# Kernel optimization log

Hardware: AMD Instinct MI355X
Metric: run time of the kernel (lower is better)

The kernel has to match this reference:

```python
import jax, jax.numpy as jnp
import numpy as np
from jax import lax

B, IMG, P, C_IN, E, H, NAX = 128, 224, 16, 1, 96, 4, 14
N = NAX * NAX  # 196 patches


def _ln(x, g, b, axes=(-1,)):
    mu = jnp.mean(x, axes, keepdims=True)
    v = jnp.var(x, axes, keepdims=True)
    return (x - mu) * lax.rsqrt(v + 1e-5) * g + b


def _embed3d(p):
    # p: [B, N, E]. Torch code rotates pair (2i,2i+1) by theta_i*col (row loop)
    # then theta_i*row (col loop) in-place => total angle theta_i*(row+col).
    bsz = p.shape[0]
    f = p.transpose(0, 2, 1).reshape(bsz, E, NAX, NAX)
    i = jnp.arange(E // 2, dtype=jnp.float32)
    theta = 10000.0 ** (-2.0 * i / E)  # [48]
    pos = jnp.arange(NAX, dtype=jnp.float32)
    ang = theta[:, None, None] * (pos[None, :, None] + pos[None, None, :])  # [48,14,14]
    cos, sin = jnp.cos(ang), jnp.sin(ang)
    xe, ye = f[:, 0::2], f[:, 1::2]  # [B,48,14,14] each
    rx = xe * cos - ye * sin
    ry = xe * sin + ye * cos
    f = jnp.stack([rx, ry], axis=2).reshape(bsz, E, NAX, NAX)  # re-interleave pairs
    return f.reshape(bsz, E, N).transpose(0, 2, 1)


def _mhsa(x, g, bt, Wqkv, bqkv, Wo, bo):
    # standard pre-norm residual MHSA block (MHSelfAttentionBlock assumed)
    h = _ln(x, g, bt)
    qkv = h @ Wqkv + bqkv  # [B,N,3E]
    q, k, v = jnp.split(qkv, 3, axis=-1)
    d = E // H
    def heads(t):
        return t.reshape(t.shape[0], N, H, d).transpose(0, 2, 1, 3)  # [B,H,N,d]
    q, k, v = heads(q), heads(k), heads(v)
    s = jnp.einsum('bhqd,bhkd->bhqk', q, k) / jnp.sqrt(jnp.float32(d))
    a = jax.nn.softmax(s, axis=-1)
    o = jnp.einsum('bhqk,bhkd->bhqd', a, v).transpose(0, 2, 1, 3).reshape(x.shape[0], N, E)
    return x + o @ Wo + bo


def _convT(x, w, b):
    # torch ConvTranspose2d(k=4, s=2, p=1); w: [C_in, C_out, 4, 4]
    wt = jnp.transpose(jnp.flip(w, (2, 3)), (1, 0, 2, 3))  # OIHW, flipped
    y = lax.conv_general_dilated(x, wt, (1, 1), ((2, 2), (2, 2)), lhs_dilation=(2, 2),
                                 dimension_numbers=('NCHW', 'OIHW', 'NCHW'))
    return y + b[None, :, None, None]


def _forward(x, timestep, Wp, bp, Wt1, bt1, Wt2, bt2,
             a0_g, a0_b, a0_Wqkv, a0_bqkv, a0_Wo, a0_bo,
             a1_g, a1_b, a1_Wqkv, a1_bqkv, a1_Wo, a1_bo,
             Wm0, bm0, Wm1, bm1, Wm2, bm2,
             Wd1, bd1, l1g, l1b, Wd2, bd2, l2g, l2b, Wd3, bd3, l3g, l3b, Wd4, bd4):
    # timestep embedding: emb = -log(0.5)*t -> [sin, cos] -> MLP
    e = 0.6931471805599453 * timestep[0]
    tv = jnp.stack([jnp.sin(e), jnp.cos(e)])  # [2]
    time = jax.nn.silu(tv @ Wt1 + bt1) @ Wt2 + bt2  # [E]
    # patch embed: conv stride 16
    p = lax.conv_general_dilated(x, Wp, (P, P), 'VALID',
                                 dimension_numbers=('NCHW', 'OIHW', 'NCHW'))
    p = (p + bp[None, :, None, None]).reshape(x.shape[0], E, N).transpose(0, 2, 1)  # [B,N,E]
    p = _embed3d(p)
    p = _mhsa(p, a0_g, a0_b, a0_Wqkv, a0_bqkv, a0_Wo, a0_bo)
    p = _mhsa(p, a1_g, a1_b, a1_Wqkv, a1_bqkv, a1_Wo, a1_bo)
    p = p + time
    p = jax.nn.silu(p @ Wm0 + bm0)
    p = jax.nn.silu(p @ Wm1 + bm1)
    p = jax.nn.silu(p @ Wm2 + bm2)
    # unpatchify decoder
    f = p.transpose(0, 2, 1).reshape(x.shape[0], E, NAX, NAX)
    f = jax.nn.silu(_ln(_convT(f, Wd1, bd1), l1g, l1b, (-2, -1)))  # [B,48,28,28]
    f = jax.nn.silu(_ln(_convT(f, Wd2, bd2), l2g, l2b, (-2, -1)))  # [B,24,56,56]
    f = jax.nn.silu(_ln(_convT(f, Wd3, bd3), l3g, l3b, (-2, -1)))  # [B,12,112,112]
    f = jax.nn.silu(_convT(f, Wd4, bd4))                            # [B,1,224,224]
    return jnp.clip(f, 0.0, 1.0)


def setup_inputs() -> dict:
    ks = jax.random.split(jax.random.key(0), 40)
    rn = lambda k, s: (jax.random.normal(k, s, jnp.float32) * 0.02)
    inp = {
        'x': jax.random.normal(ks[0], (B, C_IN, IMG, IMG), jnp.float32),
        'timestep': jax.random.uniform(ks[1], (1,), jnp.float32),
        'Wp': rn(ks[2], (E, C_IN, P, P)), 'bp': jnp.zeros((E,), jnp.float32),
        'Wt1': rn(ks[3], (2, 128)), 'bt1': jnp.zeros((128,), jnp.float32),
        'Wt2': rn(ks[4], (128, E)), 'bt2': jnp.zeros((E,), jnp.float32),
        'a0_g': jnp.ones((E,), jnp.float32), 'a0_b': jnp.zeros((E,), jnp.float32),
        'a0_Wqkv': rn(ks[5], (E, 3 * E)), 'a0_bqkv': jnp.zeros((3 * E,), jnp.float32),
        'a0_Wo': rn(ks[6], (E, E)), 'a0_bo': jnp.zeros((E,), jnp.float32),
        'a1_g': jnp.ones((E,), jnp.float32), 'a1_b': jnp.zeros((E,), jnp.float32),
        'a1_Wqkv': rn(ks[7], (E, 3 * E)), 'a1_bqkv': jnp.zeros((3 * E,), jnp.float32),
        'a1_Wo': rn(ks[8], (E, E)), 'a1_bo': jnp.zeros((E,), jnp.float32),
        'Wm0': rn(ks[9], (E, E)), 'bm0': jnp.zeros((E,), jnp.float32),
        'Wm1': rn(ks[10], (E, E)), 'bm1': jnp.zeros((E,), jnp.float32),
        'Wm2': rn(ks[11], (E, E)), 'bm2': jnp.zeros((E,), jnp.float32),
        'Wd1': rn(ks[12], (E, 48, 4, 4)), 'bd1': jnp.zeros((48,), jnp.float32),
        'l1g': jnp.ones((28, 28), jnp.float32), 'l1b': jnp.zeros((28, 28), jnp.float32),
        'Wd2': rn(ks[13], (48, 24, 4, 4)), 'bd2': jnp.zeros((24,), jnp.float32),
        'l2g': jnp.ones((56, 56), jnp.float32), 'l2b': jnp.zeros((56, 56), jnp.float32),
        'Wd3': rn(ks[14], (24, 12, 4, 4)), 'bd3': jnp.zeros((12,), jnp.float32),
        'l3g': jnp.ones((112, 112), jnp.float32), 'l3b': jnp.zeros((112, 112), jnp.float32),
        'Wd4': rn(ks[15], (12, 1, 4, 4)), 'bd4': jnp.zeros((1,), jnp.float32),
    }
    return inp


def reference(x, timestep, Wp, bp, Wt1, bt1, Wt2, bt2,
              a0_g, a0_b, a0_Wqkv, a0_bqkv, a0_Wo, a0_bo,
              a1_g, a1_b, a1_Wqkv, a1_bqkv, a1_Wo, a1_bo,
              Wm0, bm0, Wm1, bm1, Wm2, bm2,
              Wd1, bd1, l1g, l1b, Wd2, bd2, l2g, l2b, Wd3, bd3, l3g, l3b, Wd4, bd4):
    return _forward(x, timestep, Wp, bp, Wt1, bt1, Wt2, bt2,
                    a0_g, a0_b, a0_Wqkv, a0_bqkv, a0_Wo, a0_bo,
                    a1_g, a1_b, a1_Wqkv, a1_bqkv, a1_Wo, a1_bo,
                    Wm0, bm0, Wm1, bm1, Wm2, bm2,
                    Wd1, bd1, l1g, l1b, Wd2, bd2, l2g, l2b, Wd3, bd3, l3g, l3b, Wd4, bd4)
```

## Files before the change

kernel.cpp:

```cpp
#include <hip/hip_runtime.h>
#include <cmath>


#define B_   128
#define NPATCH 196
#define M_ROWS (B_*NPATCH)
#define E_   96

typedef _Float16 half8 __attribute__((ext_vector_type(8)));
typedef _Float16 half4v __attribute__((ext_vector_type(4)));
typedef float f32x4 __attribute__((ext_vector_type(4)));

__global__ void k_time(const float* __restrict__ ts,
                       const float* __restrict__ Wt1, const float* __restrict__ bt1,
                       const float* __restrict__ Wt2, const float* __restrict__ bt2,
                       float* __restrict__ timev)
{
    __shared__ float h[128];
    float e = 0.69314718055994530942f * ts[0];
    float sv = sinf(e), cv = cosf(e);
    int t = threadIdx.x;
    float z = sv * Wt1[t] + cv * Wt1[128 + t] + bt1[t];
    h[t] = z / (1.f + expf(-z));
    __syncthreads();
    if (t < 96) {
        float acc = bt2[t];
        for (int j = 0; j < 128; ++j) acc += h[j] * Wt2[j * 96 + t];
        timev[t] = acc;
    }
}

__global__ void __launch_bounds__(256) k_zstat(float* __restrict__ stat)
{
    int i = blockIdx.x * 256 + threadIdx.x;
    if (i < 21504) stat[i] = 0.f;
}

__global__ void __launch_bounds__(256) k_repack(const float* __restrict__ w1,
                                                const float* __restrict__ w2,
                                                const float* __restrict__ w3,
                                                const float* __restrict__ w4f,
                                                float* __restrict__ wr)
{
    int i = blockIdx.x * 256 + threadIdx.x;
    const float* src; int CIN, COUT, e; float* dst;
    if      (i < 73728) { src = w1;  CIN = 96; COUT = 48; e = i;          dst = wr; }
    else if (i < 92160) { src = w2;  CIN = 48; COUT = 24; e = i - 73728;  dst = wr + 73728; }
    else if (i < 96768) { src = w3;  CIN = 24; COUT = 12; e = i - 92160;  dst = wr + 92160; }
    else if (i < 96960) { src = w4f; CIN = 12; COUT = 1;  e = i - 96768;  dst = wr + 96768; }
    else return;
    int per = CIN * COUT * 4;
    int par = e / per, rem = e % per;
    int ci = rem / (COUT * 4);
    int o  = (rem >> 2) % COUT;
    int j  = rem & 3;
    int ry = par >> 1, rx = par & 1;
    int wy = (j < 2)  ? (3 - ry) : (1 - ry);
    int wx = (j & 1)  ? (1 - rx) : (3 - rx);
    dst[e] = src[(ci * COUT + o) * 16 + wy * 4 + wx];
}

__global__ void __launch_bounds__(256) k_wcvtc(const float* __restrict__ w1,
                                               _Float16* __restrict__ wc)
{
    int i = blockIdx.x * 256 + threadIdx.x;
    if (i >= 4 * 48 * 384) return;
    int p = i / 18432, rem = i % 18432;
    int o = rem / 384, k = rem % 384;
    int tap = k / 96, ci = k % 96;
    int ry = p >> 1, rx = p & 1;
    int wy = (tap < 2) ? (3 - ry) : (1 - ry);
    int wx = (tap & 1) ? (1 - rx) : (3 - rx);
    wc[i] = (_Float16)w1[(ci * 48 + o) * 16 + wy * 4 + wx];
}

__global__ void __launch_bounds__(256) k_wcvt2(const float* __restrict__ w2,
                                               _Float16* __restrict__ wc2)
{
    int i = blockIdx.x * 256 + threadIdx.x;
    if (i >= 4 * 32 * 192) return;
    int p = i / 6144, rem = i % 6144;
    int o = rem / 192, k = rem % 192;
    int tap = k / 48, ci = k % 48;
    int ry = p >> 1, rx = p & 1;
    int wy = (tap < 2) ? (3 - ry) : (1 - ry);
    int wx = (tap & 1) ? (1 - rx) : (3 - rx);
    wc2[i] = (o < 24) ? (_Float16)w2[(ci * 24 + o) * 16 + wy * 4 + wx]
                      : (_Float16)0.f;
}

__global__ void __launch_bounds__(256) k_wcvt3(const float* __restrict__ w3,
                                               _Float16* __restrict__ wc3)
{
    int i = blockIdx.x * 256 + threadIdx.x;
    if (i >= 4 * 16 * 96) return;
    int p = i / 1536, rem = i % 1536;
    int o = rem / 96, k = rem % 96;
    int tap = k / 24, ci = k % 24;
    int ry = p >> 1, rx = p & 1;
    int wy = (tap < 2) ? (3 - ry) : (1 - ry);
    int wx = (tap & 1) ? (1 - rx) : (3 - rx);
    wc3[i] = (o < 12) ? (_Float16)w3[(ci * 12 + o) * 16 + wy * 4 + wx]
                      : (_Float16)0.f;
}

__global__ void __launch_bounds__(256) k_wcvt(const float* __restrict__ qkv0,
                                              const float* __restrict__ qkv1,
                                              const float* __restrict__ wo0,
                                              const float* __restrict__ wo1,
                                              const float* __restrict__ wm0,
                                              const float* __restrict__ wm1,
                                              const float* __restrict__ wm2,
                                              _Float16* __restrict__ wh)
{
    int i = blockIdx.x * 256 + threadIdx.x;
    const float* src; int N; int e;
    if      (i < 27648)  { src = qkv0; N = 288; e = i; }
    else if (i < 55296)  { src = qkv1; N = 288; e = i - 27648; }
    else if (i < 64512)  { src = wo0;  N = 96;  e = i - 55296; }
    else if (i < 73728)  { src = wo1;  N = 96;  e = i - 64512; }
    else if (i < 82944)  { src = wm0;  N = 96;  e = i - 73728; }
    else if (i < 92160)  { src = wm1;  N = 96;  e = i - 82944; }
    else if (i < 101376) { src = wm2;  N = 96;  e = i - 92160; }
    else return;
    int n = e / 96, k = e % 96;
    wh[i] = (_Float16)src[k * N + n];
}

__global__ void __launch_bounds__(256) k_zb_h(_Float16* __restrict__ xinh)
{
    int i = blockIdx.x * 256 + threadIdx.x;
    if (i >= 128 * 60 * 96) return;
    int b = i / 5760, r = i % 5760;
    int pos = r / 96, ch = r % 96;
    int py, px;
    if      (pos < 16) { py = 0;        px = pos; }
    else if (pos < 32) { py = 15;       px = pos - 16; }
    else if (pos < 46) { py = pos - 31; px = 0; }
    else               { py = pos - 45; px = 15; }
    xinh[((size_t)(b * 256) + py * 16 + px) * 96 + ch] = (_Float16)0.f;
}

__global__ void __launch_bounds__(256) k_patch_mfma(const float* __restrict__ x,
                                                    const float* __restrict__ Wp,
                                                    const float* __restrict__ bp,
                                                    float* __restrict__ out)
{
    __shared__ __align__(16) _Float16 Ah[64 * 136];
    __shared__ __align__(16) _Float16 Wh[96 * 136];
    int t = threadIdx.x;
    int p0 = blockIdx.x * 64;
    int wave = t >> 6, lane = t & 63;
    int lm = lane & 15, quad = lane >> 4;
    f32x4 acc[6];
    #pragma unroll
    for (int nt = 0; nt < 6; ++nt) acc[nt] = (f32x4){0.f, 0.f, 0.f, 0.f};

    for (int kc = 0; kc < 2; ++kc) {
        __syncthreads();
        for (int i = t; i < 512; i += 256) {
            int lp = i >> 3, pyl = i & 7;
            int patch = p0 + lp;
            int b = patch / NPATCH, n = patch % NPATCH;
            int ny = n / 14, nx = n % 14;
            const float4* s4 = (const float4*)(x +
                ((size_t)(b * 224) + ny * 16 + kc * 8 + pyl) * 224 + nx * 16);
            float4 v0 = s4[0], v1 = s4[1], v2 = s4[2], v3 = s4[3];
            half8 h0, h1;
            h0[0]=(_Float16)v0.x; h0[1]=(_Float16)v0.y; h0[2]=(_Float16)v0.z; h0[3]=(_Float16)v0.w;
            h0[4]=(_Float16)v1.x; h0[5]=(_Float16)v1.y; h0[6]=(_Float16)v1.z; h0[7]=(_Float16)v1.w;
            h1[0]=(_Float16)v2.x; h1[1]=(_Float16)v2.y; h1[2]=(_Float16)v2.z; h1[3]=(_Float16)v2.w;
            h1[4]=(_Float16)v3.x; h1[5]=(_Float16)v3.y; h1[6]=(_Float16)v3.z; h1[7]=(_Float16)v3.w;
            *(half8*)&Ah[lp * 136 + pyl * 16]     = h0;
            *(half8*)&Ah[lp * 136 + pyl * 16 + 8] = h1;
        }
        for (int i = t; i < 1536; i += 256) {
            int e = i >> 4, s = i & 15;
            const float4* s4 = (const float4*)(Wp + e * 256 + kc * 128 + s * 8);
            float4 v0 = s4[0], v1 = s4[1];
            half8 h0;
            h0[0]=(_Float16)v0.x; h0[1]=(_Float16)v0.y; h0[2]=(_Float16)v0.z; h0[3]=(_Float16)v0.w;
            h0[4]=(_Float16)v1.x; h0[5]=(_Float16)v1.y; h0[6]=(_Float16)v1.z; h0[7]=(_Float16)v1.w;
            *(half8*)&Wh[e * 136 + s * 8] = h0;
        }
        __syncthreads();
        half8 af[4];
        #pragma unroll
        for (int ks = 0; ks < 4; ++ks)
            af[ks] = *(const half8*)&Ah[(wave * 16 + lm) * 136 + ks * 32 + quad * 8];
        #pragma unroll
        for (int ks = 0; ks < 4; ++ks) {
            #pragma unroll
            for (int nt = 0; nt < 6; ++nt) {
                half8 bf = *(const half8*)&Wh[(nt * 16 + lm) * 136 + ks * 32 + quad * 8];
                acc[nt] = __builtin_amdgcn_mfma_f32_16x16x32_f16(af[ks], bf, acc[nt], 0, 0, 0);
            }
        }
    }

    #pragma unroll
    for (int nt = 0; nt < 6; ++nt) {
        #pragma unroll
        for (int r = 0; r < 4; ++r) {
            int e = nt * 16 + lm;
            int lp = wave * 16 + quad * 4 + r;
            int patch = p0 + lp;
            int n = patch % NPATCH;
            int ny = n / 14, nx = n % 14;
            float yx = (float)(ny + nx);
            float v = acc[nt][r] + bp[e];
            float other = __shfl_xor(v, 1);
            float fi = (float)(e >> 1);
            float theta = expf(fi * (-2.f / 96.f) * 9.210340371976184f);
            float ang = theta * yx;
            float c = cosf(ang), s = sinf(ang);
            float outv = (lm & 1) ? (other * s + v * c) : (v * c - other * s);
            out[(size_t)patch * 96 + e] = outv;
        }
    }
}

__global__ void __launch_bounds__(256) k_ln_row(const float* __restrict__ x,
                                                const float* __restrict__ g,
                                                const float* __restrict__ bv,
                                                _Float16* __restrict__ out, int M)
{
    int lane = threadIdx.x & 63;
    int gw = (blockIdx.x * 256 + threadIdx.x) >> 6;
    int nw = (gridDim.x * 256) >> 6;
    float g0 = g[lane], b0 = bv[lane];
    float g1 = 0.f, b1 = 0.f;
    if (lane < 32) { g1 = g[64 + lane]; b1 = bv[64 + lane]; }
    for (int r = gw; r < M; r += nw) {
        const float* xr = x + (size_t)r * 96;
        float a = xr[lane];
        float c = (lane < 32) ? xr[64 + lane] : 0.f;
        float s = a + c, q = a * a + c * c;
        #pragma unroll
        for (int off = 32; off; off >>= 1) {
            s += __shfl_xor(s, off);
            q += __shfl_xor(q, off);
        }
        float mu = s * (1.f / 96.f);
        float rstd = rsqrtf(q * (1.f / 96.f) - mu * mu + 1e-5f);
        _Float16* orow = out + (size_t)r * 96;
        orow[lane] = (_Float16)((a - mu) * rstd * g0 + b0);
        if (lane < 32) orow[64 + lane] = (_Float16)((c - mu) * rstd * g1 + b1);
    }
}

template<int NCHUNKS, int OUTMODE, bool SILU, bool RES, bool ADDTIME, bool AHALF>
__global__ void __launch_bounds__(256) k_gemm_mfma(const void* __restrict__ A,
                                                   const _Float16* __restrict__ Wt,
                                                   const float* __restrict__ bias,
                                                   const float* __restrict__ res,
                                                   const float* __restrict__ timev,
                                                   void* __restrict__ outp)
{
    __shared__ __align__(16) _Float16 Ah[64 * 96];
    __shared__ __align__(16) _Float16 Wh[96 * 96];
    constexpr int NTOT = NCHUNKS * 96;
    int t = threadIdx.x;
    size_t row0 = (size_t)blockIdx.x * 64;

    if constexpr (AHALF) {
        const uint4* a4 = (const uint4*)((const _Float16*)A + row0 * 96);
        uint4* dst = (uint4*)Ah;
        for (int i = t; i < 768; i += 256) dst[i] = a4[i];
    } else {
        const float4* a4 = (const float4*)((const float*)A + row0 * 96);
        for (int i = t; i < 1536; i += 256) {
            float4 v = a4[i];
            half4v hv;
            hv[0] = (_Float16)v.x; hv[1] = (_Float16)v.y;
            hv[2] = (_Float16)v.z; hv[3] = (_Float16)v.w;
            *(half4v*)&Ah[i * 4] = hv;
        }
    }

    int wave = t >> 6, lane = t & 63;
    int lm = lane & 15, quad = lane >> 4;
    const f32x4 vzero = {0.f, 0.f, 0.f, 0.f};

    for (int ch = blockIdx.y; ch < NCHUNKS; ch += gridDim.y) {
        __syncthreads();
        {
            const uint4* src = (const uint4*)(Wt + (size_t)ch * 9216);
            uint4* dst = (uint4*)Wh;
            for (int i = t; i < 1152; i += 256) dst[i] = src[i];
        }
        __syncthreads();

        half8 af[3];
        #pragma unroll
        for (int ks = 0; ks < 3; ++ks)
            af[ks] = *(const half8*)&Ah[(wave * 16 + lm) * 96 + ks * 32 + quad * 8];

        f32x4 acc[6];
        #pragma unroll
        for (int ct = 0; ct < 6; ++ct) acc[ct] = vzero;

        #pragma unroll
        for (int ct = 0; ct < 6; ++ct) {
            #pragma unroll
            for (int ks = 0; ks < 3; ++ks) {
                half8 bf = *(const half8*)&Wh[(ct * 16 + lm) * 96 + ks * 32 + quad * 8];
                acc[ct] = __builtin_amdgcn_mfma_f32_16x16x32_f16(af[ks], bf, acc[ct], 0, 0, 0);
            }
        }

        #pragma unroll
        for (int ct = 0; ct < 6; ++ct) {
            #pragma unroll
            for (int r = 0; r < 4; ++r) {
                int lr = wave * 16 + quad * 4 + r;
                size_t row = row0 + lr;
                int lc = ct * 16 + lm;
                int col = ch * 96 + lc;
                float v = acc[ct][r] + bias[col];
                if constexpr (RES)     v += res[row * 96 + lc];
                if constexpr (ADDTIME) v += timev[lc];
                if constexpr (SILU)    v = v / (1.f + __expf(-v));
                if constexpr (OUTMODE == 0) {
                    ((float*)outp)[row * NTOT + col] = v;
                } else {
                    ((_Float16*)outp)[row * NTOT + col] = (_Float16)v;
                }
            }
        }
    }
}

__global__ void __launch_bounds__(256) k_mlp_fused(const float* __restrict__ A,
                                                   const _Float16* __restrict__ W,
                                                   const float* __restrict__ b0,
                                                   const float* __restrict__ b1,
                                                   const float* __restrict__ b2,
                                                   _Float16* __restrict__ outh)
{
    __shared__ __align__(16) _Float16 Ah[2][64 * 96];
    __shared__ __align__(16) _Float16 Wh[3][96 * 96];
    int t = threadIdx.x;
    size_t row0 = (size_t)blockIdx.x * 64;

    const float4* a4 = (const float4*)(A + row0 * 96);
    for (int i = t; i < 1536; i += 256) {
        float4 v = a4[i];
        half4v hv;
        hv[0] = (_Float16)v.x; hv[1] = (_Float16)v.y;
        hv[2] = (_Float16)v.z; hv[3] = (_Float16)v.w;
        *(half4v*)&Ah[0][i * 4] = hv;
    }
    {
        const uint4* src = (const uint4*)W;
        uint4* dst = (uint4*)&Wh[0][0];
        for (int i = t; i < 3456; i += 256) dst[i] = src[i];
    }

    int wave = t >> 6, lane = t & 63;
    int lm = lane & 15, quad = lane >> 4;
    const float* biases[3] = { b0, b1, b2 };
    int cur = 0;

    #pragma unroll
    for (int s = 0; s < 3; ++s) {
        __syncthreads();
        half8 af[3];
        #pragma unroll
        for (int ks = 0; ks < 3; ++ks)
            af[ks] = *(const half8*)&Ah[cur][(wave * 16 + lm) * 96 + ks * 32 + quad * 8];

        f32x4 acc[6];
        #pragma unroll
        for (int ct = 0; ct < 6; ++ct) acc[ct] = (f32x4){0.f, 0.f, 0.f, 0.f};

        #pragma unroll
        for (int ct = 0; ct < 6; ++ct) {
            #pragma unroll
            for (int ks = 0; ks < 3; ++ks) {
                half8 bf = *(const half8*)&Wh[s][(ct * 16 + lm) * 96 + ks * 32 + quad * 8];
                acc[ct] = __builtin_amdgcn_mfma_f32_16x16x32_f16(af[ks], bf, acc[ct], 0, 0, 0);
            }
        }

        const float* bias = biases[s];
        if (s < 2) {
            #pragma unroll
            for (int ct = 0; ct < 6; ++ct) {
                #pragma unroll
                for (int r = 0; r < 4; ++r) {
                    int lr = wave * 16 + quad * 4 + r;
                    int lc = ct * 16 + lm;
                    float v = acc[ct][r] + bias[lc];
                    v = v / (1.f + __expf(-v));
                    Ah[cur ^ 1][lr * 96 + lc] = (_Float16)v;
                }
            }
            cur ^= 1;
        } else {
            #pragma unroll
            for (int ct = 0; ct < 6; ++ct) {
                #pragma unroll
                for (int r = 0; r < 4; ++r) {
                    int lr = wave * 16 + quad * 4 + r;
                    size_t row = row0 + lr;
                    int lc = ct * 16 + lm;
                    float v = acc[ct][r] + bias[lc];
                    v = v / (1.f + __expf(-v));
                    size_t b = row / NPATCH; int n = (int)(row % NPATCH);
                    int ny = n / 14, nx = n % 14;
                    outh[((b * 256) + (1 + ny) * 16 + (1 + nx)) * 96 + lc] = (_Float16)v;
                }
            }
        }
    }
}

__global__ void __launch_bounds__(256) k_attn_mfma(const _Float16* __restrict__ qkv,
                                                   _Float16* __restrict__ o)
{
    __shared__ __align__(16) _Float16 Qs[208 * 40];
    __shared__ __align__(16) _Float16 Ks[208 * 40];
    __shared__ __align__(16) _Float16 Vt[32 * 232];
    __shared__ __align__(16) _Float16 Pw[4][16 * 232];

    int t = threadIdx.x;
    int bh = blockIdx.x;
    int b = bh >> 2, h = bh & 3;
    const _Float16* base = qkv + (size_t)b * NPATCH * 288 + h * 24;

    {
        const int4 z = {0, 0, 0, 0};
        int4* q4 = (int4*)Qs; int4* k4 = (int4*)Ks;
        for (int i = t; i < 1040; i += 256) { q4[i] = z; k4[i] = z; }
        int4* v4 = (int4*)Vt;
        for (int i = t; i < 928; i += 256) v4[i] = z;
        int4* p4 = (int4*)&Pw[0][0];
        for (int i = t; i < 1856; i += 256) p4[i] = z;
    }
    __syncthreads();

    for (int i = t; i < NPATCH * 24; i += 256) {
        int r = i / 24, d = i % 24;
        const _Float16* row = base + (size_t)r * 288;
        Qs[r * 40 + d]   = row[d];
        Ks[r * 40 + d]   = row[96 + d];
        Vt[d * 232 + r]  = row[192 + d];
    }
    __syncthreads();

    int wave = t >> 6, lane = t & 63;
    int lm = lane & 15, quad = lane >> 4;
    const float scale = 0.2041241452319315f;

    half8 bk[13];
    #pragma unroll
    for (int ct = 0; ct < 13; ++ct)
        bk[ct] = *(const half8*)&Ks[(ct * 16 + lm) * 40 + quad * 8];

    _Float16* pw = &Pw[wave][0];

    for (int rt = wave; rt < 13; rt += 4) {
        half8 aq = *(const half8*)&Qs[(rt * 16 + lm) * 40 + quad * 8];
        float rsum[4] = {0.f, 0.f, 0.f, 0.f};

        #pragma unroll
        for (int ct = 0; ct < 13; ++ct) {
            f32x4 s = (f32x4){0.f, 0.f, 0.f, 0.f};
            s = __builtin_amdgcn_mfma_f32_16x16x32_f16(aq, bk[ct], s, 0, 0, 0);
            #pragma unroll
            for (int r = 0; r < 4; ++r) {
                float p = __expf(fminf(s[r] * scale, 60.f));
                if (ct == 12 && lm >= 4) p = 0.f;
                rsum[r] += p;
                pw[(quad * 4 + r) * 232 + ct * 16 + lm] = (_Float16)p;
            }
        }

        #pragma unroll
        for (int r = 0; r < 4; ++r) {
            float s = rsum[r];
            s += __shfl_xor(s, 1);
            s += __shfl_xor(s, 2);
            s += __shfl_xor(s, 4);
            s += __shfl_xor(s, 8);
            rsum[r] = 1.f / s;
        }

        f32x4 ov0 = (f32x4){0.f, 0.f, 0.f, 0.f};
        f32x4 ov1 = (f32x4){0.f, 0.f, 0.f, 0.f};
        #pragma unroll
        for (int ks = 0; ks < 7; ++ks) {
            half8 ap = *(const half8*)&pw[lm * 232 + ks * 32 + quad * 8];
            half8 bv0 = *(const half8*)&Vt[(lm) * 232 + ks * 32 + quad * 8];
            half8 bv1 = *(const half8*)&Vt[(16 + lm) * 232 + ks * 32 + quad * 8];
            ov0 = __builtin_amdgcn_mfma_f32_16x16x32_f16(ap, bv0, ov0, 0, 0, 0);
            ov1 = __builtin_amdgcn_mfma_f32_16x16x32_f16(ap, bv1, ov1, 0, 0, 0);
        }

        #pragma unroll
        for (int r = 0; r < 4; ++r) {
            int row = rt * 16 + quad * 4 + r;
            if (row < NPATCH) {
                _Float16* orow = o + ((size_t)b * NPATCH + row) * 96 + h * 24;
// ... 173 lines not shown
                int pylw = pw / 28, pxw = pw % 28;
                int oy = 2 * (2 * s + pylw) + ry, ox = 2 * pxw + rx;
                _Float16* orow = c2 + ((size_t)(b * 56 + oy) * 56 + ox) * 24;
                float v0 = acc0[r] + bias[lm];
                orow[lm] = (_Float16)v0;
                s0l += v0; q0l += v0 * v0;
                if (lm < 8) {
                    float v1 = acc1[r] + bias[16 + lm];
                    orow[16 + lm] = (_Float16)v1;
                    s1l += v1; q1l += v1 * v1;
                }
            }
        }
    }
    atomicAdd(&bins[lm * 2],     s0l);
    atomicAdd(&bins[lm * 2 + 1], q0l);
    if (lm < 8) {
        atomicAdd(&bins[(16 + lm) * 2],     s1l);
        atomicAdd(&bins[(16 + lm) * 2 + 1], q1l);
    }
    __syncthreads();
    if (t < 48) atomicAdd(&pstat2[(size_t)b * 48 + t], bins[t]);
}

__global__ void __launch_bounds__(256) k_ln2_apply(const _Float16* __restrict__ c2,
                                                   const float* __restrict__ pstat2,
                                                   const float* __restrict__ g,
                                                   const float* __restrict__ bv,
                                                   _Float16* __restrict__ xh)
{
    int i4 = blockIdx.x * 256 + threadIdx.x;
    int idx = i4 * 4;
    int ch = idx % 24;
    int t2 = idx / 24;
    int pos = t2 % 3364;
    int b = t2 / 3364;
    int py = pos / 58, px = pos % 58;
    half4v hv = (half4v){(_Float16)0.f, (_Float16)0.f, (_Float16)0.f, (_Float16)0.f};
    if (py >= 1 && py <= 56 && px >= 1 && px <= 56) {
        int j = (py - 1) * 56 + (px - 1);
        half4v v = *(const half4v*)&c2[((size_t)b * 3136 + j) * 24 + ch];
        const float* ps = pstat2 + (size_t)b * 48 + ch * 2;
        float gj = g[j], bj = bv[j];
        #pragma unroll
        for (int k = 0; k < 4; ++k) {
            float mu = ps[2 * k] * (1.f / 3136.f);
            float rstd = rsqrtf(ps[2 * k + 1] * (1.f / 3136.f) - mu * mu + 1e-5f);
            float u = ((float)v[k] - mu) * rstd * gj + bj;
            hv[k] = (_Float16)(u / (1.f + __expf(-u)));
        }
    }
    *(half4v*)&xh[idx] = hv;
}

__global__ void __launch_bounds__(256) k_conv3_tile(const _Float16* __restrict__ xh,
                                                    const _Float16* __restrict__ wc,
                                                    const float* __restrict__ bias,
                                                    _Float16* __restrict__ c3,
                                                    float* __restrict__ pstat3)
{
    __shared__ __align__(16) _Float16 Xs[3 * 58 * 40];
    __shared__ float bins[24];
    int t = threadIdx.x;
    int blk = blockIdx.x;
    int b = blk / 56, s = blk % 56;

    if (t < 24) bins[t] = 0.f;

    for (int i = t; i < 522; i += 256) {
        int r = i / 174, rem = i % 174;
        int c = rem / 3, ch = (rem % 3) * 8;
        *(uint4*)&Xs[(r * 58 + c) * 40 + ch] =
            *(const uint4*)(xh + ((size_t)(b * 3364) + (s + r) * 58 + c) * 24 + ch);
    }

    int wave = t >> 6, lane = t & 63;
    int lm = lane & 15, quad = lane >> 4;
    int ry = wave >> 1, rx = wave & 1;

    half8 bf[3];
    #pragma unroll
    for (int ks = 0; ks < 3; ++ks)
        bf[ks] = *(const half8*)&wc[((size_t)(wave * 16 + lm)) * 96 + ks * 32 + quad * 8];

    __syncthreads();

    float sl = 0.f, ql = 0.f;
    #pragma unroll
    for (int rt = 0; rt < 4; ++rt) {
        int px = rt * 16 + lm;
        int pxc = px < 56 ? px : 55;

        half8 af[3];
        #pragma unroll
        for (int ks = 0; ks < 3; ++ks) {
            int k0 = ks * 32 + quad * 8;
            int tap = k0 / 24, off = k0 % 24;
            int dy = tap >> 1, dx = tap & 1;
            af[ks] = *(const half8*)&Xs[((ry + dy) * 58 + (pxc + rx + dx)) * 40 + off];
        }

        f32x4 acc = (f32x4){0.f, 0.f, 0.f, 0.f};
        #pragma unroll
        for (int ks = 0; ks < 3; ++ks)
            acc = __builtin_amdgcn_mfma_f32_16x16x32_f16(af[ks], bf[ks], acc, 0, 0, 0);

        if (lm < 12) {
            #pragma unroll
            for (int r = 0; r < 4; ++r) {
                int pw = rt * 16 + quad * 4 + r;
                if (pw < 56) {
                    int oy = 2 * s + ry, ox = 2 * pw + rx;
                    float v = acc[r] + bias[lm];
                    sl += v; ql += v * v;
                    c3[((size_t)(b * 112 + oy) * 112 + ox) * 12 + lm] = (_Float16)v;
                }
            }
        }
    }
    if (lm < 12) {
        atomicAdd(&bins[lm * 2],     sl);
        atomicAdd(&bins[lm * 2 + 1], ql);
    }
    __syncthreads();
    if (t < 24) atomicAdd(&pstat3[(size_t)b * 24 + t], bins[t]);
}

__global__ void __launch_bounds__(256) k_ln3_apply(const _Float16* __restrict__ c3,
                                                   const float* __restrict__ pstat3,
                                                   const float* __restrict__ g,
                                                   const float* __restrict__ bv,
                                                   _Float16* __restrict__ xh4)
{
    int i4 = blockIdx.x * 256 + threadIdx.x;
    int idx = i4 * 4;
    int ch = idx % 12;
    int t2 = idx / 12;
    int pix = t2 % 12544;
    int b = t2 / 12544;
    half4v v = *(const half4v*)&c3[idx];
    const float* ps = pstat3 + (size_t)b * 24 + ch * 2;
    float gp = g[pix], bp = bv[pix];
    half4v hv;
    #pragma unroll
    for (int k = 0; k < 4; ++k) {
        float mu = ps[2 * k] * (1.f / 12544.f);
        float rstd = rsqrtf(ps[2 * k + 1] * (1.f / 12544.f) - mu * mu + 1e-5f);
        float u = ((float)v[k] - mu) * rstd * gp + bp;
        hv[k] = (_Float16)(u / (1.f + __expf(-u)));
    }
    *(half4v*)&xh4[idx] = hv;
}

__global__ void __launch_bounds__(256) k_conv_final_nhwc(const _Float16* __restrict__ x,
                                                         const float* __restrict__ wr,
                                                         const float* __restrict__ bias,
                                                         float* __restrict__ out)
{
    constexpr int HIN = 112, CIN = 12;
    constexpr int NPB = (B_ * HIN * HIN) / 256;
    int pb = blockIdx.x % NPB;
    int ry = blockIdx.x / NPB;
    int rem = pb * 256 + threadIdx.x;
    int b   = rem / (HIN * HIN);
    int pix = rem % (HIN * HIN);
    int py = pix / HIN, px = pix % HIN;
    int r0 = py + ry - 1, r1 = r0 + 1;
    const _Float16* xb = x + (size_t)b * (HIN * HIN * CIN);

    int   rows[2] = { r0, r1 };
    bool  rm[2]   = { r0 >= 0, r1 < HIN };
    int   cols[3] = { px - 1, px, px + 1 };
    bool  cm[3]   = { px >= 1, true, px + 1 < HIN };

    float gv[6][12];
    #pragma unroll
    for (int a = 0; a < 2; ++a) {
        #pragma unroll
        for (int cc = 0; cc < 3; ++cc) {
            int gi = a * 3 + cc;
            if (rm[a] && cm[cc]) {
                const _Float16* p = xb + ((size_t)(rows[a] * HIN + cols[cc])) * CIN;
                half4v h0 = *(const half4v*)&p[0];
                half4v h1 = *(const half4v*)&p[4];
                half4v h2 = *(const half4v*)&p[8];
                #pragma unroll
                for (int j = 0; j < 4; ++j) {
                    gv[gi][j]     = (float)h0[j];
                    gv[gi][4 + j] = (float)h1[j];
                    gv[gi][8 + j] = (float)h2[j];
                }
            } else {
                #pragma unroll
                for (int j = 0; j < 12; ++j) gv[gi][j] = 0.f;
            }
        }
    }

    const float4* w4 = (const float4*)wr;
    float acc0 = 0.f, acc1 = 0.f;
    #pragma unroll
    for (int ci = 0; ci < CIN; ++ci) {
        float4 W0 = w4[(2 * ry) * CIN + ci];
        float4 W1 = w4[(2 * ry + 1) * CIN + ci];
        acc0 += gv[0][ci] * W0.x + gv[1][ci] * W0.y + gv[3][ci] * W0.z + gv[4][ci] * W0.w;
        acc1 += gv[1][ci] * W1.x + gv[2][ci] * W1.y + gv[4][ci] * W1.z + gv[5][ci] * W1.w;
    }

    float bb = bias[0];
    float u0 = acc0 + bb, u1 = acc1 + bb;
    u0 = u0 / (1.f + __expf(-u0));
    u1 = u1 / (1.f + __expf(-u1));
    float2 v;
    v.x = fminf(fmaxf(u0, 0.f), 1.f);
    v.y = fminf(fmaxf(u1, 0.f), 1.f);
    int oy = 2 * py + ry;
    *(float2*)(out + (size_t)b * 50176 + oy * 224 + 2 * px) = v;
}

extern "C" void kernel_launch(void* const* d_in, const int* in_sizes, int n_in,
                              void* d_out, int out_size, void* d_ws, size_t ws_size,
                              hipStream_t stream)
{
    const float* x       = (const float*)d_in[0];
    const float* ts      = (const float*)d_in[1];
    const float* Wp      = (const float*)d_in[2];
    const float* bp      = (const float*)d_in[3];
    const float* Wt1     = (const float*)d_in[4];
    const float* bt1     = (const float*)d_in[5];
    const float* Wt2     = (const float*)d_in[6];
    const float* bt2     = (const float*)d_in[7];
    const float* a0_g    = (const float*)d_in[8];
    const float* a0_b    = (const float*)d_in[9];
    const float* a0_Wqkv = (const float*)d_in[10];
    const float* a0_bqkv = (const float*)d_in[11];
    const float* a0_Wo   = (const float*)d_in[12];
    const float* a0_bo   = (const float*)d_in[13];
    const float* a1_g    = (const float*)d_in[14];
    const float* a1_b    = (const float*)d_in[15];
    const float* a1_Wqkv = (const float*)d_in[16];
    const float* a1_bqkv = (const float*)d_in[17];
    const float* a1_Wo   = (const float*)d_in[18];
    const float* a1_bo   = (const float*)d_in[19];
    const float* Wm0     = (const float*)d_in[20];
    const float* bm0     = (const float*)d_in[21];
    const float* Wm1     = (const float*)d_in[22];
    const float* bm1     = (const float*)d_in[23];
    const float* Wm2     = (const float*)d_in[24];
    const float* bm2     = (const float*)d_in[25];
    const float* Wd1     = (const float*)d_in[26];
    const float* bd1     = (const float*)d_in[27];
    const float* l1g     = (const float*)d_in[28];
    const float* l1b     = (const float*)d_in[29];
    const float* Wd2     = (const float*)d_in[30];
    const float* bd2     = (const float*)d_in[31];
    const float* l2g     = (const float*)d_in[32];
    const float* l2b     = (const float*)d_in[33];
    const float* Wd3     = (const float*)d_in[34];
    const float* bd3     = (const float*)d_in[35];
    const float* l3g     = (const float*)d_in[36];
    const float* l3b     = (const float*)d_in[37];
    const float* Wd4     = (const float*)d_in[38];
    const float* bd4     = (const float*)d_in[39];
    float* out = (float*)d_out;

    const size_t R = 2408448;
    float* ws   = (float*)d_ws;
    float* tvec = ws;
    float* p0   = ws + 512;
    _Float16* hh   = (_Float16*)(ws + 512 + R);
    _Float16* qkvh = (_Float16*)(ws + 512 + 2 * R);
    _Float16* obh  = (_Float16*)(ws + 512 + 5 * R);
    float* p1   = ws + 512 + 6 * R;
    _Float16* xinh = (_Float16*)(ws + 512 + 2 * R);
    _Float16* C1h  = (_Float16*)(ws + 512 + 5 * R);
    _Float16* xh2  = (_Float16*)(ws + 512 + 7 * R);
    _Float16* C2h  = (_Float16*)(ws + 512);
    _Float16* xh3  = (_Float16*)(ws + 512 + 7 * R + 5529600);
    _Float16* C3h  = (_Float16*)(ws + 512);
    _Float16* xh4  = (_Float16*)(ws + 512 + 7 * R + 5529600);
    float* Wr   = ws + 512 + 7 * R + 5529600 + 10334208;
    _Float16* WH = (_Float16*)(Wr + 96960);
    _Float16* Wc  = (_Float16*)Wr;
    _Float16* Wc2 = (_Float16*)(Wr + 36864);
    _Float16* Wc3 = (_Float16*)(Wr + 49152);
    float* stat = Wr + 96960 + 50688;
    float* stat1 = stat;
    float* stat2 = stat + 12288;
    float* stat3 = stat + 18432;
    const size_t NEED = (512 + 7 * R + 5529600 + 10334208 + 96960 + 50688 + 21504 + 16)
                        * sizeof(float);
    if (ws_size < NEED) return;

    _Float16* WHqkv0 = WH;
    _Float16* WHqkv1 = WH + 27648;
    _Float16* WHwo0  = WH + 55296;
    _Float16* WHwo1  = WH + 64512;
    _Float16* WHwm0  = WH + 73728;

    k_time<<<1, 128, 0, stream>>>(ts, Wt1, bt1, Wt2, bt2, tvec);
    k_zstat<<<84, 256, 0, stream>>>(stat);
    k_repack<<<379, 256, 0, stream>>>(Wd1, Wd2, Wd3, Wd4, Wr);
    k_wcvtc<<<288, 256, 0, stream>>>(Wd1, Wc);
    k_wcvt2<<<96, 256, 0, stream>>>(Wd2, Wc2);
    k_wcvt3<<<24, 256, 0, stream>>>(Wd3, Wc3);
    k_wcvt<<<396, 256, 0, stream>>>(a0_Wqkv, a1_Wqkv, a0_Wo, a1_Wo,
                                    Wm0, Wm1, Wm2, WH);
    k_patch_mfma<<<M_ROWS / 64, 256, 0, stream>>>(x, Wp, bp, p0);

    k_ln_row<<<1024, 256, 0, stream>>>(p0, a0_g, a0_b, hh, M_ROWS);
    k_gemm_mfma<3, 1, false, false, false, true><<<dim3(M_ROWS / 64, 3), 256, 0, stream>>>(
        hh, WHqkv0, a0_bqkv, nullptr, nullptr, qkvh);
    k_attn_mfma<<<B_ * 4, 256, 0, stream>>>(qkvh, obh);
    k_gemm_mfma<1, 0, false, true, false, true><<<dim3(M_ROWS / 64, 1), 256, 0, stream>>>(
        obh, WHwo0, a0_bo, p0, nullptr, p1);

    k_ln_row<<<1024, 256, 0, stream>>>(p1, a1_g, a1_b, hh, M_ROWS);
    k_gemm_mfma<3, 1, false, false, false, true><<<dim3(M_ROWS / 64, 3), 256, 0, stream>>>(
        hh, WHqkv1, a1_bqkv, nullptr, nullptr, qkvh);
    k_attn_mfma<<<B_ * 4, 256, 0, stream>>>(qkvh, obh);
    k_gemm_mfma<1, 0, false, true, true, true><<<dim3(M_ROWS / 64, 1), 256, 0, stream>>>(
        obh, WHwo1, a1_bo, p1, tvec, p0);

    k_zb_h<<<2880, 256, 0, stream>>>(xinh);

    k_mlp_fused<<<M_ROWS / 64, 256, 0, stream>>>(p0, WHwm0, bm0, bm1, bm2, xinh);

    k_conv1_tile<<<B_ * 7, 256, 0, stream>>>(xinh, Wc, bd1, C1h, stat1);
    k_ln1_apply<<<5400, 256, 0, stream>>>(C1h, stat1, l1g, l1b, xh2);
    k_conv2_tile<<<B_ * 14, 256, 0, stream>>>(xh2, Wc2, bd2, C2h, stat2);
    k_ln2_apply<<<10092, 256, 0, stream>>>(C2h, stat2, l2g, l2b, xh3);
    k_conv3_tile<<<B_ * 56, 256, 0, stream>>>(xh3, Wc3, bd3, C3h, stat3);
    k_ln3_apply<<<18816, 256, 0, stream>>>(C3h, stat3, l3g, l3b, xh4);
    k_conv_final_nhwc<<<2 * 6272, 256, 0, stream>>>(xh4, Wr + 96768, bd4, out);
}
```

Baseline: 457.7 us.

## Fuse LayerNorms into GEMM epilogues, emit fp16 MLP input, merge final conv rows

The two standalone row LayerNorm kernels go away. The first LN is computed in the patch-embed epilogue and the second in the first Wo GEMM epilogue, using 16-lane shuffle reductions over the 96 columns. The last Wo GEMM now writes fp16 so the MLP kernel copies its input directly instead of converting from fp32. The final transposed conv computes both output rows per thread from a 3x3 input neighbourhood, which halves the grid and the repeated input loads. This saves two launches and several full-activation read/write passes, at the cost of more registers in the epilogues and fp16 rounding of the MLP input.

```diff
diff --git a/kernel.cpp b/kernel.cpp
--- a/kernel.cpp
+++ b/kernel.cpp
@@ -144,12 +144,15 @@
 __global__ void __launch_bounds__(256) k_patch_mfma(const float* __restrict__ x,
                                                     const float* __restrict__ Wp,
                                                     const float* __restrict__ bp,
-                                                    float* __restrict__ out)
+                                                    const float* __restrict__ lng,
+                                                    const float* __restrict__ lnb,
+                                                    float* __restrict__ out,
+                                                    _Float16* __restrict__ outh)
 {
     __shared__ __align__(16) _Float16 Ah[64 * 136];
     __shared__ __align__(16) _Float16 Wh[96 * 136];
     int t = threadIdx.x;
-    int p0 = blockIdx.x * 64;
+    int pb = blockIdx.x * 64;
     int wave = t >> 6, lane = t & 63;
     int lm = lane & 15, quad = lane >> 4;
     f32x4 acc[6];
@@ -160,7 +163,7 @@
         __syncthreads();
         for (int i = t; i < 512; i += 256) {
             int lp = i >> 3, pyl = i & 7;
-            int patch = p0 + lp;
+            int patch = pb + lp;
             int b = patch / NPATCH, n = patch % NPATCH;
             int ny = n / 14, nx = n % 14;
             const float4* s4 = (const float4*)(x +
@@ -198,13 +201,15 @@
         }
     }
 
+    float vv[6][4];
+    float sr[4] = {0.f, 0.f, 0.f, 0.f}, qr[4] = {0.f, 0.f, 0.f, 0.f};
     #pragma unroll
     for (int nt = 0; nt < 6; ++nt) {
         #pragma unroll
         for (int r = 0; r < 4; ++r) {
             int e = nt * 16 + lm;
             int lp = wave * 16 + quad * 4 + r;
-            int patch = p0 + lp;
+            int patch = pb + lp;
             int n = patch % NPATCH;
             int ny = n / 14, nx = n % 14;
             float yx = (float)(ny + nx);
@@ -215,47 +220,46 @@
             float ang = theta * yx;
             float c = cosf(ang), s = sinf(ang);
             float outv = (lm & 1) ? (other * s + v * c) : (v * c - other * s);
-            out[(size_t)patch * 96 + e] = outv;
-        }
-    }
-}
-
-__global__ void __launch_bounds__(256) k_ln_row(const float* __restrict__ x,
-                                                const float* __restrict__ g,
-                                                const float* __restrict__ bv,
-                                                _Float16* __restrict__ out, int M)
-{
-    int lane = threadIdx.x & 63;
-    int gw = (blockIdx.x * 256 + threadIdx.x) >> 6;
-    int nw = (gridDim.x * 256) >> 6;
-    float g0 = g[lane], b0 = bv[lane];
-    float g1 = 0.f, b1 = 0.f;
-    if (lane < 32) { g1 = g[64 + lane]; b1 = bv[64 + lane]; }
-    for (int r = gw; r < M; r += nw) {
-        const float* xr = x + (size_t)r * 96;
-        float a = xr[lane];
-        float c = (lane < 32) ? xr[64 + lane] : 0.f;
-        float s = a + c, q = a * a + c * c;
-        #pragma unroll
-        for (int off = 32; off; off >>= 1) {
-            s += __shfl_xor(s, off);
-            q += __shfl_xor(q, off);
-        }
+            vv[nt][r] = outv;
+            sr[r] += outv; qr[r] += outv * outv;
+        }
+    }
+    float mur[4], rsr[4];
+    #pragma unroll
+    for (int r = 0; r < 4; ++r) {
+        float s = sr[r], q = qr[r];
+        s += __shfl_xor(s, 1); q += __shfl_xor(q, 1);
+        s += __shfl_xor(s, 2); q += __shfl_xor(q, 2);
+        s += __shfl_xor(s, 4); q += __shfl_xor(q, 4);
+        s += __shfl_xor(s, 8); q += __shfl_xor(q, 8);
         float mu = s * (1.f / 96.f);
-        float rstd = rsqrtf(q * (1.f / 96.f) - mu * mu + 1e-5f);
-        _Float16* orow = out + (size_t)r * 96;
-        orow[lane] = (_Float16)((a - mu) * rstd * g0 + b0);
-        if (lane < 32) orow[64 + lane] = (_Float16)((c - mu) * rstd * g1 + b1);
-    }
-}
-
-template<int NCHUNKS, int OUTMODE, bool SILU, bool RES, bool ADDTIME, bool AHALF>
+        mur[r] = mu;
+        rsr[r] = rsqrtf(q * (1.f / 96.f) - mu * mu + 1e-5f);
+    }
+    #pragma unroll
+    for (int nt = 0; nt < 6; ++nt) {
+        #pragma unroll
+        for (int r = 0; r < 4; ++r) {
+            int e = nt * 16 + lm;
+            int lp = wave * 16 + quad * 4 + r;
+            size_t patch = (size_t)(pb + lp);
+            out[patch * 96 + e] = vv[nt][r];
+            outh[patch * 96 + e] =
+                (_Float16)((vv[nt][r] - mur[r]) * rsr[r] * lng[e] + lnb[e]);
+        }
+    }
+}
+
+template<int NCHUNKS, int OUTMODE, bool SILU, bool RES, bool ADDTIME, bool AHALF, bool LNF>
 __global__ void __launch_bounds__(256) k_gemm_mfma(const void* __restrict__ A,
                                                    const _Float16* __restrict__ Wt,
                                                    const float* __restrict__ bias,
                                                    const float* __restrict__ res,
                                                    const float* __restrict__ timev,
-                                                   void* __restrict__ outp)
+                                                   void* __restrict__ outp,
+                                                   const float* __restrict__ lng,
+                                                   const float* __restrict__ lnb,
+                                                   _Float16* __restrict__ outh2)
 {
     __shared__ __align__(16) _Float16 Ah[64 * 96];
     __shared__ __align__(16) _Float16 Wh[96 * 96];
@@ -309,29 +313,72 @@
             }
         }
 
-        #pragma unroll
-        for (int ct = 0; ct < 6; ++ct) {
+        if constexpr (LNF) {
+            float vv[6][4];
+            float sr[4] = {0.f, 0.f, 0.f, 0.f}, qr[4] = {0.f, 0.f, 0.f, 0.f};
+            #pragma unroll
+            for (int ct = 0; ct < 6; ++ct) {
+                #pragma unroll
+                for (int r = 0; r < 4; ++r) {
+                    int lr = wave * 16 + quad * 4 + r;
+                    size_t row = row0 + lr;
+                    int lc = ct * 16 + lm;
+                    float v = acc[ct][r] + bias[lc];
+                    if constexpr (RES)     v += res[row * 96 + lc];
+                    if constexpr (ADDTIME) v += timev[lc];
+                    vv[ct][r] = v;
+                    sr[r] += v; qr[r] += v * v;
+                }
+            }
+            float mur[4], rsr[4];
             #pragma unroll
             for (int r = 0; r < 4; ++r) {
-                int lr = wave * 16 + quad * 4 + r;
-                size_t row = row0 + lr;
-                int lc = ct * 16 + lm;
-                int col = ch * 96 + lc;
-                float v = acc[ct][r] + bias[col];
-                if constexpr (RES)     v += res[row * 96 + lc];
-                if constexpr (ADDTIME) v += timev[lc];
-                if constexpr (SILU)    v = v / (1.f + __expf(-v));
-                if constexpr (OUTMODE == 0) {
-                    ((float*)outp)[row * NTOT + col] = v;
-                } else {
-                    ((_Float16*)outp)[row * NTOT + col] = (_Float16)v;
+                float s = sr[r], q = qr[r];
+                s += __shfl_xor(s, 1); q += __shfl_xor(q, 1);
+                s += __shfl_xor(s, 2); q += __shfl_xor(q, 2);
+                s += __shfl_xor(s, 4); q += __shfl_xor(q, 4);
+                s += __shfl_xor(s, 8); q += __shfl_xor(q, 8);
+                float mu = s * (1.f / 96.f);
+                mur[r] = mu;
+                rsr[r] = rsqrtf(q * (1.f / 96.f) - mu * mu + 1e-5f);
+            }
+            #pragma unroll
+            for (int ct = 0; ct < 6; ++ct) {
+                #pragma unroll
+                for (int r = 0; r < 4; ++r) {
+                    int lr = wave * 16 + quad * 4 + r;
+                    size_t row = row0 + lr;
+                    int lc = ct * 16 + lm;
+                    ((float*)outp)[row * 96 + lc] = vv[ct][r];
+                    outh2[row * 96 + lc] =
+                        (_Float16)((vv[ct][r] - mur[r]) * rsr[r] * lng[lc] + lnb[lc]);
                 }
             }
-        }
-    }
-}
-
-__global__ void __launch_bounds__(256) k_mlp_fused(const float* __restrict__ A,
+        } else {
+            #pragma unroll
+            for (int ct = 0; ct < 6; ++ct) {
+                #pragma unroll
+                for (int r = 0; r < 4; ++r) {
+                    int lr = wave * 16 + quad * 4 + r;
+                    size_t row = row0 + lr;
+                    int lc = ct * 16 + lm;
+                    int col = ch * 96 + lc;
+                    float v = acc[ct][r] + bias[col];
+                    if constexpr (RES)     v += res[row * 96 + lc];
+                    if constexpr (ADDTIME) v += timev[lc];
+                    if constexpr (SILU)    v = v / (1.f + __expf(-v));
+                    if constexpr (OUTMODE == 0) {
+                        ((float*)outp)[row * NTOT + col] = v;
+                    } else {
+                        ((_Float16*)outp)[row * NTOT + col] = (_Float16)v;
+                    }
+                }
+            }
+        }
+    }
+}
+
+__global__ void __launch_bounds__(256) k_mlp_fused(const _Float16* __restrict__ A,
                                                    const _Float16* __restrict__ W,
                                                    const float* __restrict__ b0,
                                                    const float* __restrict__ b1,
@@ -343,13 +390,10 @@
     int t = threadIdx.x;
     size_t row0 = (size_t)blockIdx.x * 64;
 
-    const float4* a4 = (const float4*)(A + row0 * 96);
-    for (int i = t; i < 1536; i += 256) {
-        float4 v = a4[i];
-        half4v hv;
-        hv[0] = (_Float16)v.x; hv[1] = (_Float16)v.y;
-        hv[2] = (_Float16)v.z; hv[3] = (_Float16)v.w;
-        *(half4v*)&Ah[0][i * 4] = hv;
+    {
+        const uint4* a4 = (const uint4*)(A + row0 * 96);
+        uint4* dst = (uint4*)&Ah[0][0];
+        for (int i = t; i < 768; i += 256) dst[i] = a4[i];
     }
     {
         const uint4* src = (const uint4*)W;
@@ -829,70 +873,83 @@
     *(half4v*)&xh4[idx] = hv;
 }
 
-__global__ void __launch_bounds__(256) k_conv_final_nhwc(const _Float16* __restrict__ x,
-                                                         const float* __restrict__ wr,
-                                                         const float* __restrict__ bias,
-                                                         float* __restrict__ out)
+__global__ void __launch_bounds__(256) k_conv_final2(const _Float16* __restrict__ x,
+                                                     const float* __restrict__ wr,
+                                                     const float* __restrict__ bias,
+                                                     float* __restrict__ out)
 {
     constexpr int HIN = 112, CIN = 12;
-    constexpr int NPB = (B_ * HIN * HIN) / 256;
-    int pb = blockIdx.x % NPB;
-    int ry = blockIdx.x / NPB;
-    int rem = pb * 256 + threadIdx.x;
+    int rem = blockIdx.x * 256 + threadIdx.x;
     int b   = rem / (HIN * HIN);
     int pix = rem % (HIN * HIN);
     int py = pix / HIN, px = pix % HIN;
-    int r0 = py + ry - 1, r1 = r0 + 1;
     const _Float16* xb = x + (size_t)b * (HIN * HIN * CIN);
-
-    int   rows[2] = { r0, r1 };
-    bool  rm[2]   = { r0 >= 0, r1 < HIN };
-    int   cols[3] = { px - 1, px, px + 1 };
-    bool  cm[3]   = { px >= 1, true, px + 1 < HIN };
-
-    float gv[6][12];
-    #pragma unroll
-    for (int a = 0; a < 2; ++a) {
-        #pragma unroll
-        for (int cc = 0; cc < 3; ++cc) {
-            int gi = a * 3 + cc;
-            if (rm[a] && cm[cc]) {
-                const _Float16* p = xb + ((size_t)(rows[a] * HIN + cols[cc])) * CIN;
+    const float4* w4 = (const float4*)wr;
+
+    float acc00 = 0.f, acc01 = 0.f, acc10 = 0.f, acc11 = 0.f;
+
+    #pragma unroll
+    for (int a = 0; a < 3; ++a) {
+        int row = py - 1 + a;
+        bool rv = (a == 1) || (row >= 0 && row < HIN);
+        #pragma unroll
+        for (int c = 0; c < 3; ++c) {
+            int col = px - 1 + c;
+            bool cv = (c == 1) || (col >= 0 && col < HIN);
+            float tv[12];
+            if (rv && cv) {
+                const _Float16* p = xb + ((size_t)(row * HIN + col)) * CIN;
                 half4v h0 = *(const half4v*)&p[0];
                 half4v h1 = *(const half4v*)&p[4];
                 half4v h2 = *(const half4v*)&p[8];
                 #pragma unroll
                 for (int j = 0; j < 4; ++j) {
-                    gv[gi][j]     = (float)h0[j];
-                    gv[gi][4 + j] = (float)h1[j];
-                    gv[gi][8 + j] = (float)h2[j];
+                    tv[j]     = (float)h0[j];
+                    tv[4 + j] = (float)h1[j];
+                    tv[8 + j] = (float)h2[j];
                 }
             } else {
                 #pragma unroll
-                for (int j = 0; j < 12; ++j) gv[gi][j] = 0.f;
-            }
-        }
-    }
-
-    const float4* w4 = (const float4*)wr;
-    float acc0 = 0.f, acc1 = 0.f;
-    #pragma unroll
-    for (int ci = 0; ci < CIN; ++ci) {
-        float4 W0 = w4[(2 * ry) * CIN + ci];
-        float4 W1 = w4[(2 * ry + 1) * CIN + ci];
-        acc0 += gv[0][ci] * W0.x + gv[1][ci] * W0.y + gv[3][ci] * W0.z + gv[4][ci] * W0.w;
-        acc1 += gv[1][ci] * W1.x + gv[2][ci] * W1.y + gv[4][ci] * W1.z + gv[5][ci] * W1.w;
+                for (int j = 0; j < 12; ++j) tv[j] = 0.f;
+            }
+            #pragma unroll
+            for (int ry = 0; ry < 2; ++ry) {
+                int dy = a - ry;
+                if (dy < 0 || dy > 1) continue;
+                #pragma unroll
+                for (int rx = 0; rx < 2; ++rx) {
+                    int dx = c - rx;
+                    if (dx < 0 || dx > 1) continue;
+                    int j = dy * 2 + dx;
+                    const float4* wp = w4 + (ry * 2 + rx) * 12;
+                    float sacc = 0.f;
+                    #pragma unroll
+                    for (int ci = 0; ci < 12; ++ci) {
+                        float4 W = wp[ci];
+                        float wj = (j == 0) ? W.x : (j == 1) ? W.y : (j == 2) ? W.z : W.w;
+                        sacc += tv[ci] * wj;
+                    }
+                    if (ry == 0) { if (rx == 0) acc00 += sacc; else acc01 += sacc; }
+                    else         { if (rx == 0) acc10 += sacc; else acc11 += sacc; }
+                }
+            }
+        }
     }
 
     float bb = bias[0];
-    float u0 = acc0 + bb, u1 = acc1 + bb;
-    u0 = u0 / (1.f + __expf(-u0));
-    u1 = u1 / (1.f + __expf(-u1));
-    float2 v;
-    v.x = fminf(fmaxf(u0, 0.f), 1.f);
-    v.y = fminf(fmaxf(u1, 0.f), 1.f);
-    int oy = 2 * py + ry;
-    *(float2*)(out + (size_t)b * 50176 + oy * 224 + 2 * px) = v;
+    float u00 = acc00 + bb, u01 = acc01 + bb, u10 = acc10 + bb, u11 = acc11 + bb;
+    u00 = u00 / (1.f + __expf(-u00));
+    u01 = u01 / (1.f + __expf(-u01));
+    u10 = u10 / (1.f + __expf(-u10));
+    u11 = u11 / (1.f + __expf(-u11));
+    float2 v0, v1;
+    v0.x = fminf(fmaxf(u00, 0.f), 1.f);
+    v0.y = fminf(fmaxf(u01, 0.f), 1.f);
+    v1.x = fminf(fmaxf(u10, 0.f), 1.f);
+    v1.y = fminf(fmaxf(u11, 0.f), 1.f);
+    float* ob = out + (size_t)b * 50176;
+    *(float2*)(ob + (2 * py) * 224 + 2 * px)     = v0;
+    *(float2*)(ob + (2 * py + 1) * 224 + 2 * px) = v1;
 }
 
 extern "C" void kernel_launch(void* const* d_in, const int* in_sizes, int n_in,
@@ -945,6 +1002,7 @@
     float* ws   = (float*)d_ws;
     float* tvec = ws;
     float* p0   = ws + 512;
+    _Float16* p0h  = (_Float16*)(ws + 512);
     _Float16* hh   = (_Float16*)(ws + 512 + R);
     _Float16* qkvh = (_Float16*)(ws + 512 + 2 * R);
     _Float16* obh  = (_Float16*)(ws + 512 + 5 * R);
@@ -983,25 +1041,27 @@
     k_wcvt3<<<24, 256, 0, stream>>>(Wd3, Wc3);
     k_wcvt<<<396, 256, 0, stream>>>(a0_Wqkv, a1_Wqkv, a0_Wo, a1_Wo,
                                     Wm0, Wm1, Wm2, WH);
-    k_patch_mfma<<<M_ROWS / 64, 256, 0, stream>>>(x, Wp, bp, p0);
-
-    k_ln_row<<<1024, 256, 0, stream>>>(p0, a0_g, a0_b, hh, M_ROWS);
-    k_gemm_mfma<3, 1, false, false, false, true><<<dim3(M_ROWS / 64, 3), 256, 0, stream>>>(
-        hh, WHqkv0, a0_bqkv, nullptr, nullptr, qkvh);
+    k_patch_mfma<<<M_ROWS / 64, 256, 0, stream>>>(x, Wp, bp, a0_g, a0_b, p0, hh);
+
+    k_gemm_mfma<3, 1, false, false, false, true, false>
+        <<<dim3(M_ROWS / 64, 3), 256, 0, stream>>>(
+        hh, WHqkv0, a0_bqkv, nullptr, nullptr, qkvh, nullptr, nullptr, nullptr);
     k_attn_mfma<<<B_ * 4, 256, 0, stream>>>(qkvh, obh);
-    k_gemm_mfma<1, 0, false, true, false, true><<<dim3(M_ROWS / 64, 1), 256, 0, stream>>>(
-        obh, WHwo0, a0_bo, p0, nullptr, p1);
-
-    k_ln_row<<<1024, 256, 0, stream>>>(p1, a1_g, a1_b, hh, M_ROWS);
-    k_gemm_mfma<3, 1, false, false, false, true><<<dim3(M_ROWS / 64, 3), 256, 0, stream>>>(
-        hh, WHqkv1, a1_bqkv, nullptr, nullptr, qkvh);
+    k_gemm_mfma<1, 0, false, true, false, true, true>
+        <<<dim3(M_ROWS / 64, 1), 256, 0, stream>>>(
+        obh, WHwo0, a0_bo, p0, nullptr, p1, a1_g, a1_b, hh);
+
+    k_gemm_mfma<3, 1, false, false, false, true, false>
+        <<<dim3(M_ROWS / 64, 3), 256, 0, stream>>>(
+        hh, WHqkv1, a1_bqkv, nullptr, nullptr, qkvh, nullptr, nullptr, nullptr);
     k_attn_mfma<<<B_ * 4, 256, 0, stream>>>(qkvh, obh);
-    k_gemm_mfma<1, 0, false, true, true, true><<<dim3(M_ROWS / 64, 1), 256, 0, stream>>>(
-        obh, WHwo1, a1_bo, p1, tvec, p0);
+    k_gemm_mfma<1, 1, false, true, true, true, false>
+        <<<dim3(M_ROWS / 64, 1), 256, 0, stream>>>(
+        obh, WHwo1, a1_bo, p1, tvec, p0h, nullptr, nullptr, nullptr);
 
     k_zb_h<<<2880, 256, 0, stream>>>(xinh);
 
-    k_mlp_fused<<<M_ROWS / 64, 256, 0, stream>>>(p0, WHwm0, bm0, bm1, bm2, xinh);
+    k_mlp_fused<<<M_ROWS / 64, 256, 0, stream>>>(p0h, WHwm0, bm0, bm1, bm2, xinh);
 
     k_conv1_tile<<<B_ * 7, 256, 0, stream>>>(xinh, Wc, bd1, C1h, stat1);
     k_ln1_apply<<<5400, 256, 0, stream>>>(C1h, stat1, l1g, l1b, xh2);
@@ -1009,5 +1069,5 @@
     k_ln2_apply<<<10092, 256, 0, stream>>>(C2h, stat2, l2g, l2b, xh3);
     k_conv3_tile<<<B_ * 56, 256, 0, stream>>>(xh3, Wc3, bd3, C3h, stat3);
     k_ln3_apply<<<18816, 256, 0, stream>>>(C3h, stat3, l3g, l3b, xh4);
-    k_conv_final_nhwc<<<2 * 6272, 256, 0, stream>>>(xh4, Wr + 96768, bd4, out);
-}
+    k_conv_final2<<<6272, 256, 0, stream>>>(xh4, Wr + 96768, bd4, out);
+}
```

Result: slower. 508.7 us (+11.1%).
